# Kernel optimization log

Hardware: AMD Instinct MI355X
Metric: run time of the kernel (lower is better)

The kernel has to match this reference:

```python
import math
import jax, jax.numpy as jnp
import numpy as np

B, H, HKV, L, S, D = 1, 32, 8, 2048, 2048, 128
N_REP = H // HKV          # 4
SCALE = 1.0 / math.sqrt(D)


def setup_inputs() -> dict:
    key = jax.random.key(0)
    k1, k2, k3, k4 = jax.random.split(key, 4)
    query = jax.random.normal(k1, (B, H, L, D), dtype=jnp.float32)
    k_ = jax.random.normal(k2, (B, HKV, S, D), dtype=jnp.float32)
    v_ = jax.random.normal(k3, (B, HKV, S, D), dtype=jnp.float32)
    attn_mask = jax.random.normal(k4, (B, 1, L, S), dtype=jnp.float32)
    return {"query": query, "key": k_, "value": v_, "attn_mask": attn_mask}


def reference(query, key, value, attn_mask):
    # repeat_kv: Q -> [B, HKV, n_rep, L, D]; K/V stay [B, HKV, S, D]
    # (the torch code reshapes K/V to [B, HKV, 1, S, D]; broadcasting via
    # einsum is equivalent), mask unsqueezed at dim 1 -> [B, 1, 1, L, S].
    q = query.reshape(B, HKV, N_REP, L, D)
    scores = jnp.einsum("bkrld,bksd->bkrls", q, key)          # [B,HKV,n_rep,L,S]
    scores = scores + attn_mask[:, None]                        # broadcast add
    # softmax_fp8(x, dim=-1, invAttnHead=1/sqrt(D)) scales input by invAttnHead
    w = jax.nn.softmax(scores * SCALE, axis=-1)
    # dropout_p = 0.0 -> identity
    out = jnp.einsum("bkrls,bksd->bkrld", w, value)             # [B,HKV,n_rep,L,D]
    return out
```

## Files before the change

### kernel.cpp

```cpp
#include <hip/hip_runtime.h>

#define NH   32
#define NKV  8
#define LQ   2048
#define SK   2048
#define DH   128
#define BM   128
#define BN   64
#define KSTRIDE 136
#define VSTRIDE 72
#define PSTRIDE 72

typedef __attribute__((ext_vector_type(8)))  short bf8;
typedef __attribute__((ext_vector_type(4)))  float f4;
typedef __attribute__((ext_vector_type(16))) float f16v;

#if __has_builtin(__builtin_amdgcn_exp2f)
#define EXP2F(x) __builtin_amdgcn_exp2f(x)
#else
#define EXP2F(x) exp2f(x)
#endif

__device__ __forceinline__ unsigned short f2bf(float f) {
    unsigned int u = __builtin_bit_cast(unsigned int, f);
    u = (u + 0x7FFFu + ((u >> 16) & 1u)) >> 16;
    return (unsigned short)u;
}

__global__ __launch_bounds__(256) void convert_k_kernel(
    const float* __restrict__ K, unsigned short* __restrict__ Kb)
{
    size_t base = ((size_t)blockIdx.x * 256 + threadIdx.x) * 8;
    float4 a = *(const float4*)(K + base);
    float4 b = *(const float4*)(K + base + 4);
    bf8 o;
    o[0] = (short)f2bf(a.x); o[1] = (short)f2bf(a.y);
    o[2] = (short)f2bf(a.z); o[3] = (short)f2bf(a.w);
    o[4] = (short)f2bf(b.x); o[5] = (short)f2bf(b.y);
    o[6] = (short)f2bf(b.z); o[7] = (short)f2bf(b.w);
    *(bf8*)(Kb + base) = o;
}

__global__ __launch_bounds__(256) void transpose_v_kernel(
    const float* __restrict__ V, unsigned short* __restrict__ VTb)
{
    __shared__ __align__(16) unsigned short Vl[DH * VSTRIDE];
    const int tid = threadIdx.x;
    const int kv  = blockIdx.x >> 5;
    const int s0  = (blockIdx.x & 31) * 64;
    const float* Vh = V + (size_t)kv * SK * DH;

    #pragma unroll
    for (int i = 0; i < 8; ++i) {
        int idx = tid * 4 + i * 1024;
        int s = idx >> 7, d = idx & 127;
        const float4 v4 = *(const float4*)(Vh + (size_t)(s0 + s) * DH + d);
        Vl[(d + 0) * VSTRIDE + s] = f2bf(v4.x);
        Vl[(d + 1) * VSTRIDE + s] = f2bf(v4.y);
        Vl[(d + 2) * VSTRIDE + s] = f2bf(v4.z);
        Vl[(d + 3) * VSTRIDE + s] = f2bf(v4.w);
    }
    __syncthreads();
    unsigned short* out = VTb + (size_t)kv * DH * SK;
    #pragma unroll
    for (int i = 0; i < 4; ++i) {
        int c = tid + i * 256;
        int d = c >> 3, s8 = (c & 7) * 8;
        *(bf8*)(out + (size_t)d * SK + s0 + s8) = *(const bf8*)(Vl + d * VSTRIDE + s8);
    }
}

__global__ __launch_bounds__(256, 2) void fattn_kernel(
    const float* __restrict__ Q, const unsigned short* __restrict__ Kb,
    const unsigned short* __restrict__ VTb, const float* __restrict__ M,
    float* __restrict__ O)
{
    __shared__ __align__(16) unsigned short Klds[BN * KSTRIDE];
    __shared__ __align__(16) unsigned short Vlds[DH * VSTRIDE];
    __shared__ __align__(16) unsigned short Plds[4 * 32 * PSTRIDE];

    const int tid  = threadIdx.x;
    const int wave = tid >> 6;
    const int lane = tid & 63;
    const int l32  = lane & 31;
    const int hh   = lane >> 5;

    const int bx = blockIdx.x;
    const int h  = bx >> 4;
    const int lt = bx & 15;
    const int q0 = lt * BM;
    const int kv = h >> 2;

    const float*          Qh  = Q   + (size_t)h  * LQ * DH;
    const unsigned short* Kh  = Kb  + (size_t)kv * SK * DH;
    const unsigned short* VTh = VTb + (size_t)kv * DH * SK;

    const int sK0 = tid >> 4,        dK0 = (tid & 15) * 8;
    const int dV0 = tid >> 3,        sV0 = (tid & 7) * 8;

    const int qrow = q0 + wave * 32 + l32;
    const float* Mq = M + (size_t)qrow * SK;

    bf8 bQ[8];
    #pragma unroll
    for (int ks = 0; ks < 8; ++ks) {
        const float* qp = Qh + (size_t)qrow * DH + ks * 16 + hh * 8;
        float4 a = *(const float4*)(qp);
        float4 b = *(const float4*)(qp + 4);
        bQ[ks][0] = (short)f2bf(a.x); bQ[ks][1] = (short)f2bf(a.y);
        bQ[ks][2] = (short)f2bf(a.z); bQ[ks][3] = (short)f2bf(a.w);
        bQ[ks][4] = (short)f2bf(b.x); bQ[ks][5] = (short)f2bf(b.y);
        bQ[ks][6] = (short)f2bf(b.z); bQ[ks][7] = (short)f2bf(b.w);
    }

    f16v accO[4];
    #pragma unroll
    for (int nt = 0; nt < 4; ++nt)
        #pragma unroll
        for (int r = 0; r < 16; ++r) accO[nt][r] = 0.f;
    float lpart = 0.f;

    const float scale_log2e = 0.08838834764831845f * 1.4426950408889634f;

    unsigned short* Pw = Plds + wave * 32 * PSTRIDE;

    bf8 kf[4], vf[4];
    #pragma unroll
    for (int c = 0; c < 4; ++c) {
        kf[c] = *(const bf8*)(Kh + (size_t)(sK0 + c * 16) * DH + dK0);
        vf[c] = *(const bf8*)(VTh + (size_t)(dV0 + c * 32) * SK + sV0);
    }

    for (int s0i = 0; s0i < SK; s0i += BN) {
        __syncthreads();
        #pragma unroll
        for (int c = 0; c < 4; ++c) {
            *(bf8*)(Klds + (sK0 + c * 16) * KSTRIDE + dK0) = kf[c];
            *(bf8*)(Vlds + (dV0 + c * 32) * VSTRIDE + sV0) = vf[c];
        }
        __syncthreads();
        if (s0i + BN < SK) {
            #pragma unroll
            for (int c = 0; c < 4; ++c) {
                kf[c] = *(const bf8*)(Kh + (size_t)(s0i + BN + sK0 + c * 16) * DH + dK0);
                vf[c] = *(const bf8*)(VTh + (size_t)(dV0 + c * 32) * SK + s0i + BN + sV0);
            }
        }
        float4 mv[2][4];
        #pragma unroll
        for (int mt = 0; mt < 2; ++mt)
            #pragma unroll
            for (int grp = 0; grp < 4; ++grp)
                mv[mt][grp] = *(const float4*)(Mq + s0i + mt * 32 + grp * 8 + hh * 4);

        f16v accS[2];
        #pragma unroll
        for (int mt = 0; mt < 2; ++mt) {
            f16v a;
            #pragma unroll
            for (int r = 0; r < 16; ++r) a[r] = 0.f;
            #pragma unroll
            for (int ks = 0; ks < 8; ++ks) {
                bf8 aK = *(const bf8*)(Klds + (mt * 32 + l32) * KSTRIDE + ks * 16 + hh * 8);
                a = __builtin_amdgcn_mfma_f32_32x32x16_bf16(aK, bQ[ks], a, 0, 0, 0);
            }
            accS[mt] = a;
        }

        #pragma unroll
        for (int mt = 0; mt < 2; ++mt) {
            #pragma unroll
            for (int grp = 0; grp < 4; ++grp) {
                ushort4 pk;
                float e0 = EXP2F((accS[mt][grp * 4 + 0] + mv[mt][grp].x) * scale_log2e);
                float e1 = EXP2F((accS[mt][grp * 4 + 1] + mv[mt][grp].y) * scale_log2e);
                float e2 = EXP2F((accS[mt][grp * 4 + 2] + mv[mt][grp].z) * scale_log2e);
                float e3 = EXP2F((accS[mt][grp * 4 + 3] + mv[mt][grp].w) * scale_log2e);
                lpart += (e0 + e1) + (e2 + e3);
                pk.x = f2bf(e0); pk.y = f2bf(e1); pk.z = f2bf(e2); pk.w = f2bf(e3);
                *(ushort4*)(Pw + l32 * PSTRIDE + mt * 32 + grp * 8 + hh * 4) = pk;
            }
        }
        asm volatile("s_waitcnt lgkmcnt(0)" ::: "memory");

        bf8 bP[4];
        #pragma unroll
        for (int ks = 0; ks < 4; ++ks)
            bP[ks] = *(const bf8*)(Pw + l32 * PSTRIDE + ks * 16 + hh * 8);
        #pragma unroll
        for (int nt = 0; nt < 4; ++nt) {
            f16v a = accO[nt];
            #pragma unroll
            for (int ks = 0; ks < 4; ++ks) {
                bf8 aV = *(const bf8*)(Vlds + (nt * 32 + l32) * VSTRIDE + ks * 16 + hh * 8);
                a = __builtin_amdgcn_mfma_f32_32x32x16_bf16(aV, bP[ks], a, 0, 0, 0);
            }
            accO[nt] = a;
        }
    }

    float l = lpart + __shfl_xor(lpart, 32);
    float inv = 1.0f / l;
    float* Op = O + (size_t)h * LQ * DH + (size_t)qrow * DH;
    #pragma unroll
    for (int nt = 0; nt < 4; ++nt) {
        #pragma unroll
        for (int grp = 0; grp < 4; ++grp) {
            int d = nt * 32 + grp * 8 + hh * 4;
            float4 o;
            o.x = accO[nt][grp * 4 + 0] * inv;
            o.y = accO[nt][grp * 4 + 1] * inv;
            o.z = accO[nt][grp * 4 + 2] * inv;
            o.w = accO[nt][grp * 4 + 3] * inv;
            *(float4*)(Op + d) = o;
        }
    }
}

extern "C" void kernel_launch(void* const* d_in, const int* in_sizes, int n_in,
                              void* d_out, int out_size, void* d_ws, size_t ws_size,
                              hipStream_t stream) {
    const float* Q = (const float*)d_in[0];
    const float* K = (const float*)d_in[1];
    const float* V = (const float*)d_in[2];
    const float* M = (const float*)d_in[3];
    float* O = (float*)d_out;

    unsigned short* Kb  = (unsigned short*)d_ws;
    unsigned short* VTb = Kb + (size_t)NKV * SK * DH;

    convert_k_kernel<<<dim3((NKV * SK * DH) / (256 * 8)), 256, 0, stream>>>(K, Kb);
    transpose_v_kernel<<<dim3(NKV * (SK / 64)), 256, 0, stream>>>(V, VTb);

    dim3 grid(NH * (LQ / BM));
    fattn_kernel<<<grid, 256, 0, stream>>>(Q, Kb, VTb, M, O);
}
```

Measured before the change: 200.7 us.

## Double-buffer K/V LDS tiles and pass P via lane shuffles instead of LDS

Uses two LDS buffers for K and V so the next tile's shared-memory store happens after the QK^T MFMAs, dropping one of the two barriers per iteration. Separately, it removes the per-wave P scratch in LDS. The bf16 probabilities are packed into registers and exchanged between the half-waves with __shfl_xor to build the B operand of the PV MFMA. This cuts LDS round-trips and the extra waitcnt, but adds shuffle instructions and more LDS for the doubled K/V buffers, which may affect occupancy at two blocks per CU.

```diff
diff --git a/kernel.cpp b/kernel.cpp
--- a/kernel.cpp
+++ b/kernel.cpp
@@ -9,7 +9,6 @@
 #define BN   64
 #define KSTRIDE 136
 #define VSTRIDE 72
-#define PSTRIDE 72
 
 typedef __attribute__((ext_vector_type(8)))  short bf8;
 typedef __attribute__((ext_vector_type(4)))  float f4;
@@ -21,10 +20,10 @@
 #define EXP2F(x) exp2f(x)
 #endif
 
-__device__ __forceinline__ unsigned short f2bf(float f) {
+__device__ __forceinline__ unsigned int f2bf(float f) {
     unsigned int u = __builtin_bit_cast(unsigned int, f);
     u = (u + 0x7FFFu + ((u >> 16) & 1u)) >> 16;
-    return (unsigned short)u;
+    return u;
 }
 
 __global__ __launch_bounds__(256) void convert_k_kernel(
@@ -55,10 +54,10 @@
         int idx = tid * 4 + i * 1024;
         int s = idx >> 7, d = idx & 127;
         const float4 v4 = *(const float4*)(Vh + (size_t)(s0 + s) * DH + d);
-        Vl[(d + 0) * VSTRIDE + s] = f2bf(v4.x);
-        Vl[(d + 1) * VSTRIDE + s] = f2bf(v4.y);
-        Vl[(d + 2) * VSTRIDE + s] = f2bf(v4.z);
-        Vl[(d + 3) * VSTRIDE + s] = f2bf(v4.w);
+        Vl[(d + 0) * VSTRIDE + s] = (unsigned short)f2bf(v4.x);
+        Vl[(d + 1) * VSTRIDE + s] = (unsigned short)f2bf(v4.y);
+        Vl[(d + 2) * VSTRIDE + s] = (unsigned short)f2bf(v4.z);
+        Vl[(d + 3) * VSTRIDE + s] = (unsigned short)f2bf(v4.w);
     }
     __syncthreads();
     unsigned short* out = VTb + (size_t)kv * DH * SK;
@@ -75,9 +74,8 @@
     const unsigned short* __restrict__ VTb, const float* __restrict__ M,
     float* __restrict__ O)
 {
-    __shared__ __align__(16) unsigned short Klds[BN * KSTRIDE];
-    __shared__ __align__(16) unsigned short Vlds[DH * VSTRIDE];
-    __shared__ __align__(16) unsigned short Plds[4 * 32 * PSTRIDE];
+    __shared__ __align__(16) unsigned short Klds[2][BN * KSTRIDE];
+    __shared__ __align__(16) unsigned short Vlds[2][DH * VSTRIDE];
 
     const int tid  = threadIdx.x;
     const int wave = tid >> 6;
@@ -122,30 +120,27 @@
 
     const float scale_log2e = 0.08838834764831845f * 1.4426950408889634f;
 
-    unsigned short* Pw = Plds + wave * 32 * PSTRIDE;
-
     bf8 kf[4], vf[4];
     #pragma unroll
     for (int c = 0; c < 4; ++c) {
         kf[c] = *(const bf8*)(Kh + (size_t)(sK0 + c * 16) * DH + dK0);
         vf[c] = *(const bf8*)(VTh + (size_t)(dV0 + c * 32) * SK + sV0);
     }
-
-    for (int s0i = 0; s0i < SK; s0i += BN) {
+    #pragma unroll
+    for (int c = 0; c < 4; ++c) {
+        *(bf8*)(&Klds[0][(sK0 + c * 16) * KSTRIDE + dK0]) = kf[c];
+        *(bf8*)(&Vlds[0][(dV0 + c * 32) * VSTRIDE + sV0]) = vf[c];
+    }
+    #pragma unroll
+    for (int c = 0; c < 4; ++c) {
+        kf[c] = *(const bf8*)(Kh + (size_t)(BN + sK0 + c * 16) * DH + dK0);
+        vf[c] = *(const bf8*)(VTh + (size_t)(dV0 + c * 32) * SK + BN + sV0);
+    }
+
+    int buf = 0;
+    for (int s0i = 0; s0i < SK; s0i += BN, buf ^= 1) {
         __syncthreads();
-        #pragma unroll
-        for (int c = 0; c < 4; ++c) {
-            *(bf8*)(Klds + (sK0 + c * 16) * KSTRIDE + dK0) = kf[c];
-            *(bf8*)(Vlds + (dV0 + c * 32) * VSTRIDE + sV0) = vf[c];
-        }
-        __syncthreads();
-        if (s0i + BN < SK) {
-            #pragma unroll
-            for (int c = 0; c < 4; ++c) {
-                kf[c] = *(const bf8*)(Kh + (size_t)(s0i + BN + sK0 + c * 16) * DH + dK0);
-                vf[c] = *(const bf8*)(VTh + (size_t)(dV0 + c * 32) * SK + s0i + BN + sV0);
-            }
-        }
+
         float4 mv[2][4];
         #pragma unroll
         for (int mt = 0; mt < 2; ++mt)
@@ -153,6 +148,8 @@
             for (int grp = 0; grp < 4; ++grp)
                 mv[mt][grp] = *(const float4*)(Mq + s0i + mt * 32 + grp * 8 + hh * 4);
 
+        const unsigned short* Kc = Klds[buf];
+        const unsigned short* Vc = Vlds[buf];
         f16v accS[2];
         #pragma unroll
         for (int mt = 0; mt < 2; ++mt) {
@@ -161,38 +158,68 @@
             for (int r = 0; r < 16; ++r) a[r] = 0.f;
             #pragma unroll
             for (int ks = 0; ks < 8; ++ks) {
-                bf8 aK = *(const bf8*)(Klds + (mt * 32 + l32) * KSTRIDE + ks * 16 + hh * 8);
+                bf8 aK = *(const bf8*)(Kc + (mt * 32 + l32) * KSTRIDE + ks * 16 + hh * 8);
                 a = __builtin_amdgcn_mfma_f32_32x32x16_bf16(aK, bQ[ks], a, 0, 0, 0);
             }
             accS[mt] = a;
         }
 
+        if (s0i + BN < SK) {
+            #pragma unroll
+            for (int c = 0; c < 4; ++c) {
+                *(bf8*)(&Klds[buf ^ 1][(sK0 + c * 16) * KSTRIDE + dK0]) = kf[c];
+                *(bf8*)(&Vlds[buf ^ 1][(dV0 + c * 32) * VSTRIDE + sV0]) = vf[c];
+            }
+            if (s0i + 2 * BN < SK) {
+                #pragma unroll
+                for (int c = 0; c < 4; ++c) {
+                    kf[c] = *(const bf8*)(Kh + (size_t)(s0i + 2 * BN + sK0 + c * 16) * DH + dK0);
+                    vf[c] = *(const bf8*)(VTh + (size_t)(dV0 + c * 32) * SK + s0i + 2 * BN + sV0);
+                }
+            }
+        }
+
+        unsigned int W[2][4][2];
         #pragma unroll
         for (int mt = 0; mt < 2; ++mt) {
             #pragma unroll
-            for (int grp = 0; grp < 4; ++grp) {
-                ushort4 pk;
-                float e0 = EXP2F((accS[mt][grp * 4 + 0] + mv[mt][grp].x) * scale_log2e);
-                float e1 = EXP2F((accS[mt][grp * 4 + 1] + mv[mt][grp].y) * scale_log2e);
-                float e2 = EXP2F((accS[mt][grp * 4 + 2] + mv[mt][grp].z) * scale_log2e);
-                float e3 = EXP2F((accS[mt][grp * 4 + 3] + mv[mt][grp].w) * scale_log2e);
+            for (int g = 0; g < 4; ++g) {
+                float e0 = EXP2F((accS[mt][g * 4 + 0] + mv[mt][g].x) * scale_log2e);
+                float e1 = EXP2F((accS[mt][g * 4 + 1] + mv[mt][g].y) * scale_log2e);
+                float e2 = EXP2F((accS[mt][g * 4 + 2] + mv[mt][g].z) * scale_log2e);
+                float e3 = EXP2F((accS[mt][g * 4 + 3] + mv[mt][g].w) * scale_log2e);
                 lpart += (e0 + e1) + (e2 + e3);
-                pk.x = f2bf(e0); pk.y = f2bf(e1); pk.z = f2bf(e2); pk.w = f2bf(e3);
-                *(ushort4*)(Pw + l32 * PSTRIDE + mt * 32 + grp * 8 + hh * 4) = pk;
-            }
-        }
-        asm volatile("s_waitcnt lgkmcnt(0)" ::: "memory");
+                W[mt][g][0] = f2bf(e0) | (f2bf(e1) << 16);
+                W[mt][g][1] = f2bf(e2) | (f2bf(e3) << 16);
+            }
+        }
+        unsigned int R[2][4][2];
+        #pragma unroll
+        for (int mt = 0; mt < 2; ++mt)
+            #pragma unroll
+            for (int g = 0; g < 4; ++g)
+                #pragma unroll
+                for (int b = 0; b < 2; ++b)
+                    R[mt][g][b] = (unsigned int)__shfl_xor((int)W[mt][g][b], 32);
 
         bf8 bP[4];
         #pragma unroll
-        for (int ks = 0; ks < 4; ++ks)
-            bP[ks] = *(const bf8*)(Pw + l32 * PSTRIDE + ks * 16 + hh * 8);
+        for (int ks = 0; ks < 4; ++ks) {
+            const int mt = ks >> 1, b = (ks & 1) * 2;
+            unsigned int lo0 = hh ? R[mt][b + 1][0] : W[mt][b][0];
+            unsigned int lo1 = hh ? R[mt][b + 1][1] : W[mt][b][1];
+            unsigned int hi0 = hh ? W[mt][b + 1][0] : R[mt][b][0];
+            unsigned int hi1 = hh ? W[mt][b + 1][1] : R[mt][b][1];
+            uint4 u = {lo0, lo1, hi0, hi1};
+            bP[ks] = __builtin_bit_cast(bf8, u);
+        }
+
         #pragma unroll
         for (int nt = 0; nt < 4; ++nt) {
             f16v a = accO[nt];
             #pragma unroll
             for (int ks = 0; ks < 4; ++ks) {
-                bf8 aV = *(const bf8*)(Vlds + (nt * 32 + l32) * VSTRIDE + ks * 16 + hh * 8);
+                bf8 aV = *(const bf8*)(Vc + (nt * 32 + l32) * VSTRIDE + ks * 16 + hh * 8);
                 a = __builtin_amdgcn_mfma_f32_32x32x16_bf16(aV, bP[ks], a, 0, 0, 0);
             }
             accO[nt] = a;
```

New measurement: 202.5 us. About the same (+0.9%).
